# Performance work log

Measured on AMD Instinct MI355X. Metric: run time of the kernel, lower is better.

Reference implementation:

```python
import jax, jax.numpy as jnp
import numpy as np

H = 64; W = 64; P = 16; NPH = 4; NPW = 4; PH = 16; PW = 16; ZD = 32; HD = 1024; UD = 3; B = 256


def affine_grid(theta, Ho, Wo):
    # torch F.affine_grid, align_corners=False. theta [N,2,3] -> grid [N,Ho,Wo,2]
    xs = (2.0 * jnp.arange(Wo, dtype=theta.dtype) + 1.0) / Wo - 1.0
    ys = (2.0 * jnp.arange(Ho, dtype=theta.dtype) + 1.0) / Ho - 1.0
    X, Y = jnp.meshgrid(xs, ys)  # [Ho,Wo] each, x varies along last axis
    base = jnp.stack([X, Y, jnp.ones_like(X)], axis=-1)  # [Ho,Wo,3]
    return jnp.einsum('nij,hwj->nhwi', theta, base)


def grid_sample(img, grid):
    # torch F.grid_sample bilinear, padding_mode='zeros', align_corners=False
    # img [N,H,W], grid [N,Ho,Wo,2] in [-1,1]
    Hi, Wi = img.shape[1], img.shape[2]
    x = (grid[..., 0] + 1.0) * Wi / 2.0 - 0.5
    y = (grid[..., 1] + 1.0) * Hi / 2.0 - 0.5
    x0 = jnp.floor(x); y0 = jnp.floor(y)
    wx = x - x0; wy = y - y0

    def gather(ix, iy):
        valid = (ix >= 0) & (ix < Wi) & (iy >= 0) & (iy < Hi)
        ixc = jnp.clip(ix, 0, Wi - 1).astype(jnp.int32)
        iyc = jnp.clip(iy, 0, Hi - 1).astype(jnp.int32)
        v = jax.vmap(lambda im, yy, xx: im[yy, xx])(img, iyc, ixc)
        return jnp.where(valid, v, 0.0)

    return (gather(x0, y0) * (1 - wx) * (1 - wy)
            + gather(x0 + 1, y0) * wx * (1 - wy)
            + gather(x0, y0 + 1) * (1 - wx) * wy
            + gather(x0 + 1, y0 + 1) * wx * wy)


def rot_tr(u):
    # rotTrMatrix: u [N,3] (angle, tx, ty) -> [N,2,3]
    c = jnp.cos(u[:, 0]); s = jnp.sin(u[:, 0])
    R = jnp.stack([jnp.stack([c, -s], -1), jnp.stack([s, c], -1)], -2)  # [N,2,2]
    return jnp.concatenate([R, u[:, 1:3, None]], axis=2)


def anchor_theta():
    # anchor_move: identity rotation + per-part grid-cell-center translations
    tx = (np.arange(NPW) * (W / NPW) + W / NPW / 2) / W - 0.5
    ty = (np.arange(NPH) * (H / NPH) + H / NPH / 2) / H - 0.5
    th = np.tile(np.concatenate([np.eye(2), np.zeros((2, 1))], axis=1)[None], (P, 1, 1)).astype(np.float32)
    for k in range(P):
        th[k, 0, 2] = tx[k % NPW]
        th[k, 1, 2] = ty[k // NPW]
    return jnp.asarray(th)


def forward(inputs, W1, b1, W2, b2, Wum, bum, Wuv, buv, Wgm, bgm, Wgv, bgv, Wz, M, eps_u, eps_g):
    hid = jax.nn.relu(inputs.reshape(-1, H * W) @ W1 + b1)
    hid = jax.nn.relu(hid @ W2 + b2)
    # global transform distribution (note: F.threshold(x,-6,6) -> 6 where x<=-6)
    gmu = jnp.tanh(hid @ Wgm + bgm)
    gpre = hid @ Wgv + bgv
    gvar = jnp.exp(jnp.where(gpre > -6.0, gpre, 6.0))
    gu = gmu + gvar * eps_g  # sample_u uses mu + var*eps (var, not std) as in source
    # per-part transform distribution (F.threshold(x,-6,-6) -> clamp below at -6)
    umu = jnp.tanh(hid @ Wum + bum)
    upre = hid @ Wuv + buv
    uvar = jnp.exp(jnp.where(upre > -6.0, upre, -6.0))
    u = (umu + uvar * eps_u).reshape(-1, UD)  # [B*P,3]
    # decode parts (input is ones, as in source)
    parts = jax.nn.sigmoid(jnp.ones((B, ZD), inputs.dtype) @ Wz).reshape(B * P, PH, PW)
    padh = (H - PH) // 2; padw = (W - PW) // 2
    parts = jnp.pad(parts, ((0, 0), (padh, H - PH - padh), (padw, W - PW - padw)))
    # anchor placement of parts and kernel masks
    th_a = jnp.tile(anchor_theta(), (B, 1, 1))  # [B*P,2,3], part-minor ordering
    g_a = affine_grid(th_a, H, W)
    parts = grid_sample(parts, g_a)                     # [B*P,H,W]
    KM = grid_sample(M[:B * P].reshape(B * P, H, W), g_a)
    # per-part rotation+translation for parts; translation-only for kernel
    theta = rot_tr(u)                                   # [B*P,2,3]
    g = affine_grid(theta, H, W)
    eye = jnp.broadcast_to(jnp.eye(2, dtype=theta.dtype), (B * P, 2, 2))
    theta_K = jnp.concatenate([eye, theta[:, :, 2:3]], axis=2)
    g_K = affine_grid(theta_K, H, W)
    KM = grid_sample(KM, g_K).reshape(B, P, H, W)
    xp = grid_sample(parts, g).reshape(B, P, H, W)
    # masked weighted compositing
    num = jnp.sum(xp * KM, axis=1)
    den = jnp.sum(KM, axis=1)
    den = jnp.where(den == 0.0, 1.0, den)
    x = num / den
    # global transform
    theta_g = rot_tr(gu)
    g_g = affine_grid(theta_g, H, W)
    return grid_sample(x, g_g)[:, None]  # [B,1,H,W]


def setup_inputs() -> dict:
    key = jax.random.key(0)
    ks = jax.random.split(key, 18)

    def lin(k, fin, fout):
        return jax.random.normal(k, (fin, fout), jnp.float32) / np.sqrt(fin)

    return {
        'inputs': jax.random.uniform(ks[0], (B, H * W), jnp.float32),
        'W1': lin(ks[1], H * W, HD), 'b1': jnp.zeros((HD,), jnp.float32),
        'W2': lin(ks[2], HD, HD), 'b2': jnp.zeros((HD,), jnp.float32),
        'Wum': lin(ks[3], HD, P * UD), 'bum': jnp.zeros((P * UD,), jnp.float32),
        'Wuv': lin(ks[4], HD, P * UD), 'buv': jnp.zeros((P * UD,), jnp.float32),
        'Wgm': lin(ks[5], HD, UD), 'bgm': jnp.zeros((UD,), jnp.float32),
        'Wgv': lin(ks[6], HD, UD), 'bgv': jnp.zeros((UD,), jnp.float32),
        'Wz': lin(ks[7], ZD, P * PH * PW),
        'M': jax.random.uniform(ks[8], (B * P, 1, H, W), jnp.float32),
        'eps_u': jax.random.normal(ks[9], (B, P * UD), jnp.float32),
        'eps_g': jax.random.normal(ks[10], (B, UD), jnp.float32),
    }


def reference(inputs, W1, b1, W2, b2, Wum, bum, Wuv, buv, Wgm, bgm, Wgv, bgv, Wz, M, eps_u, eps_g):
    return forward(inputs, W1, b1, W2, b2, Wum, bum, Wuv, buv, Wgm, bgm, Wgv, bgv, Wz, M, eps_u, eps_g)
```

## Files before the change

### kernel.cpp

```cpp
#include <hip/hip_runtime.h>
#include <math.h>

#define SPLITK 8

typedef __bf16 bf16x8 __attribute__((ext_vector_type(8)));
typedef float  f32x4  __attribute__((ext_vector_type(4)));

__device__ inline unsigned short bf16rne(float x) {
    unsigned int u = __float_as_uint(x);
    unsigned int r = u + 0x7FFFu + ((u >> 16) & 1u);
    return (unsigned short)(r >> 16);
}
__device__ inline float bf16tof(unsigned short h) {
    return __uint_as_float(((unsigned int)h) << 16);
}

__global__ __launch_bounds__(256) void prep_all(
    const float* __restrict__ inputs,
    const float* __restrict__ W1, const float* __restrict__ W2,
    const float* __restrict__ Wum, const float* __restrict__ Wuv,
    const float* __restrict__ Wgm, const float* __restrict__ Wgv,
    const float* __restrict__ Wz,
    unsigned short* __restrict__ Ahi, unsigned short* __restrict__ Alo,
    unsigned short* __restrict__ W1Thi, unsigned short* __restrict__ W1Tlo,
    unsigned short* __restrict__ W2Thi, unsigned short* __restrict__ W2Tlo,
    float* __restrict__ WT, float* __restrict__ partsb)
{
    __shared__ float t[32][33];
    int bid = blockIdx.x;
    int tid = threadIdx.x;
    if (bid < 4096 || (bid >= 8192 && bid < 9216)) {
        const float* W = (bid < 4096) ? W1 : W2;
        unsigned short* Thi = (bid < 4096) ? W1Thi : W2Thi;
        unsigned short* Tlo = (bid < 4096) ? W1Tlo : W2Tlo;
        int K = (bid < 4096) ? 4096 : 1024;
        int b2 = (bid < 4096) ? bid : (bid - 8192);
        int n0 = (b2 & 31) * 32, k0 = (b2 >> 5) * 32;
        int c = tid & 31, r0 = tid >> 5;
#pragma unroll
        for (int i = 0; i < 4; i++)
            t[r0 + 8 * i][c] = W[(size_t)(k0 + r0 + 8 * i) * 1024 + n0 + c];
        __syncthreads();
        int kk = tid & 31, n1 = tid >> 5;
#pragma unroll
        for (int i = 0; i < 4; i++) {
            float x = t[kk][n1 + 8 * i];
            unsigned short h = bf16rne(x);
            unsigned short l = bf16rne(x - bf16tof(h));
            size_t o = (size_t)(n0 + n1 + 8 * i) * K + k0 + kk;
            Thi[o] = h;
            Tlo[o] = l;
        }
    } else if (bid < 8192) {
        int id = (bid - 4096) * 256 + tid;
        float x = inputs[id];
        unsigned short h = bf16rne(x);
        Ahi[id] = h;
        Alo[id] = bf16rne(x - bf16tof(h));
    } else if (bid < 9624) {
        int id = (bid - 9216) * 256 + tid;
        int o = id >> 10;
        int k = id & 1023;
        float v;
        if (o < 48)       v = Wum[k * 48 + o];
        else if (o < 96)  v = Wuv[k * 48 + (o - 48)];
        else if (o < 99)  v = Wgm[k * 3 + (o - 96)];
        else              v = Wgv[k * 3 + (o - 99)];
        WT[id] = v;
    } else {
        int idx = (bid - 9624) * 256 + tid;
        float s = 0.f;
#pragma unroll
        for (int z = 0; z < 32; z++) s += Wz[z * 4096 + idx];
        partsb[idx] = 1.f / (1.f + expf(-s));
    }
}

__global__ __launch_bounds__(256) void gemm_bf16x3(
    const unsigned short* __restrict__ Ahi, const unsigned short* __restrict__ Alo,
    const unsigned short* __restrict__ Bhi, const unsigned short* __restrict__ Blo,
    float* __restrict__ psum, int K, int kchunk)
{
    __shared__ unsigned short Ah[4096], Al[4096], Bh[4096], Bl[4096];
    int tid = threadIdx.x;
    int n0 = blockIdx.x * 64, m0 = blockIdx.y * 64;
    int kb = blockIdx.z * kchunk;
    int wid = tid >> 6, lane = tid & 63;
    int wm = wid & 1, wn = wid >> 1;
    int lm = lane & 15, q = lane >> 4;

    int r0 = tid >> 3, ch0 = tid & 7;
    int r1 = (tid + 256) >> 3, ch1 = (tid + 256) & 7;
    int l0 = r0 * 64 + 8 * (ch0 ^ (r0 & 7));
    int l1 = r1 * 64 + 8 * (ch1 ^ (r1 & 7));
    size_t ga0 = (size_t)(m0 + r0) * K + kb + ch0 * 8;
    size_t ga1 = (size_t)(m0 + r1) * K + kb + ch1 * 8;
    size_t gb0 = (size_t)(n0 + r0) * K + kb + ch0 * 8;
    size_t gb1 = (size_t)(n0 + r1) * K + kb + ch1 * 8;

    f32x4 acc[2][2] = {};

    int nkt = kchunk >> 6;
    uint4 vah0, vah1, val0, val1, vbh0, vbh1, vbl0, vbl1;
    vah0 = *(const uint4*)(Ahi + ga0);
    vah1 = *(const uint4*)(Ahi + ga1);
    val0 = *(const uint4*)(Alo + ga0);
    val1 = *(const uint4*)(Alo + ga1);
    vbh0 = *(const uint4*)(Bhi + gb0);
    vbh1 = *(const uint4*)(Bhi + gb1);
    vbl0 = *(const uint4*)(Blo + gb0);
    vbl1 = *(const uint4*)(Blo + gb1);

    int frm0 = (wm * 32 + lm) * 64;
    int frm1 = (wm * 32 + 16 + lm) * 64;
    int frn0 = (wn * 32 + lm) * 64;
    int frn1 = (wn * 32 + 16 + lm) * 64;
    int sw = lm & 7;

    for (int kt = 0; kt < nkt; kt++) {
        __syncthreads();
        *(uint4*)(Ah + l0) = vah0;
        *(uint4*)(Ah + l1) = vah1;
        *(uint4*)(Al + l0) = val0;
        *(uint4*)(Al + l1) = val1;
        *(uint4*)(Bh + l0) = vbh0;
        *(uint4*)(Bh + l1) = vbh1;
        *(uint4*)(Bl + l0) = vbl0;
        *(uint4*)(Bl + l1) = vbl1;
        __syncthreads();
        if (kt + 1 < nkt) {
            size_t o = (size_t)(kt + 1) * 64;
            vah0 = *(const uint4*)(Ahi + ga0 + o);
            vah1 = *(const uint4*)(Ahi + ga1 + o);
            val0 = *(const uint4*)(Alo + ga0 + o);
            val1 = *(const uint4*)(Alo + ga1 + o);
            vbh0 = *(const uint4*)(Bhi + gb0 + o);
            vbh1 = *(const uint4*)(Bhi + gb1 + o);
            vbl0 = *(const uint4*)(Blo + gb0 + o);
            vbl1 = *(const uint4*)(Blo + gb1 + o);
        }
#pragma unroll
        for (int ks = 0; ks < 2; ks++) {
            int cidx = 8 * (((ks << 2) + q) ^ sw);
            bf16x8 ah0 = *(const bf16x8*)(Ah + frm0 + cidx);
            bf16x8 ah1 = *(const bf16x8*)(Ah + frm1 + cidx);
            bf16x8 al0 = *(const bf16x8*)(Al + frm0 + cidx);
            bf16x8 al1 = *(const bf16x8*)(Al + frm1 + cidx);
            bf16x8 bh0 = *(const bf16x8*)(Bh + frn0 + cidx);
            bf16x8 bh1 = *(const bf16x8*)(Bh + frn1 + cidx);
            bf16x8 bl0 = *(const bf16x8*)(Bl + frn0 + cidx);
            bf16x8 bl1 = *(const bf16x8*)(Bl + frn1 + cidx);
            acc[0][0] = __builtin_amdgcn_mfma_f32_16x16x32_bf16(ah0, bh0, acc[0][0], 0, 0, 0);
            acc[0][0] = __builtin_amdgcn_mfma_f32_16x16x32_bf16(ah0, bl0, acc[0][0], 0, 0, 0);
            acc[0][0] = __builtin_amdgcn_mfma_f32_16x16x32_bf16(al0, bh0, acc[0][0], 0, 0, 0);
            acc[0][1] = __builtin_amdgcn_mfma_f32_16x16x32_bf16(ah0, bh1, acc[0][1], 0, 0, 0);
            acc[0][1] = __builtin_amdgcn_mfma_f32_16x16x32_bf16(ah0, bl1, acc[0][1], 0, 0, 0);
            acc[0][1] = __builtin_amdgcn_mfma_f32_16x16x32_bf16(al0, bh1, acc[0][1], 0, 0, 0);
            acc[1][0] = __builtin_amdgcn_mfma_f32_16x16x32_bf16(ah1, bh0, acc[1][0], 0, 0, 0);
            acc[1][0] = __builtin_amdgcn_mfma_f32_16x16x32_bf16(ah1, bl0, acc[1][0], 0, 0, 0);
            acc[1][0] = __builtin_amdgcn_mfma_f32_16x16x32_bf16(al1, bh0, acc[1][0], 0, 0, 0);
            acc[1][1] = __builtin_amdgcn_mfma_f32_16x16x32_bf16(ah1, bh1, acc[1][1], 0, 0, 0);
            acc[1][1] = __builtin_amdgcn_mfma_f32_16x16x32_bf16(ah1, bl1, acc[1][1], 0, 0, 0);
            acc[1][1] = __builtin_amdgcn_mfma_f32_16x16x32_bf16(al1, bh1, acc[1][1], 0, 0, 0);
        }
    }

    float* op = psum + (size_t)blockIdx.z * (256 * 1024);
#pragma unroll
    for (int mt = 0; mt < 2; mt++)
#pragma unroll
        for (int nt = 0; nt < 2; nt++) {
            int row = m0 + wm * 32 + mt * 16 + q * 4;
            int col = n0 + wn * 32 + nt * 16 + lm;
#pragma unroll
            for (int r = 0; r < 4; r++)
                op[(size_t)(row + r) * 1024 + col] = acc[mt][nt][r];
        }
}

__global__ __launch_bounds__(256) void reduce_bias_relu(
    const float* __restrict__ psum, const float* __restrict__ bias,
    float* __restrict__ out)
{
    int i = blockIdx.x * 256 + threadIdx.x;
    float v = 0.f;
#pragma unroll
    for (int s = 0; s < SPLITK; s++) v += psum[(size_t)s * 262144 + i];
    v += bias[i & 1023];
    out[i] = fmaxf(v, 0.f);
}

__global__ __launch_bounds__(256) void reduce_bias_relu_split(
    const float* __restrict__ psum, const float* __restrict__ bias,
    unsigned short* __restrict__ hi, unsigned short* __restrict__ lo)
{
    int i = blockIdx.x * 256 + threadIdx.x;
    float v = 0.f;
#pragma unroll
    for (int s = 0; s < SPLITK; s++) v += psum[(size_t)s * 262144 + i];
    v += bias[i & 1023];
    v = fmaxf(v, 0.f);
    unsigned short h = bf16rne(v);
    hi[i] = h;
    lo[i] = bf16rne(v - bf16tof(h));
}

__global__ __launch_bounds__(512) void heads_v2(
    const float* __restrict__ hid, const float* __restrict__ WT,
    const float* __restrict__ bum, const float* __restrict__ buv,
    const float* __restrict__ bgm, const float* __restrict__ bgv,
    const float* __restrict__ eps_u, const float* __restrict__ eps_g,
    float* __restrict__ u_out, float* __restrict__ gu_out)
{
    int b = blockIdx.x;
    int tid = threadIdx.x;
    int w = tid >> 6, l = tid & 63;

    const float* hp = hid + b * 1024 + l * 4;
    float4 hr[4];
#pragma unroll
    for (int i = 0; i < 4; i++) hr[i] = *(const float4*)(hp + i * 256);

    int o = w;
    int rm = (o < 48) ? o : (48 + o);
    int rv = (o < 48) ? (o + 48) : (51 + o);
    float4 wm[4], wv[4];
    {
        const float* wp = WT + rm * 1024 + l * 4;
#pragma unroll
        for (int i = 0; i < 4; i++) wm[i] = *(const float4*)(wp + i * 256);
        wp = WT + rv * 1024 + l * 4;
#pragma unroll
        for (int i = 0; i < 4; i++) wv[i] = *(const float4*)(wp + i * 256);
    }

    while (o < 51) {
        int onext = o + 8;
        float4 wmn[4], wvn[4];
        if (onext < 51) {
            int rm2 = (onext < 48) ? onext : (48 + onext);
            int rv2 = (onext < 48) ? (onext + 48) : (51 + onext);
            const float* wp = WT + rm2 * 1024 + l * 4;
#pragma unroll
            for (int i = 0; i < 4; i++) wmn[i] = *(const float4*)(wp + i * 256);
            wp = WT + rv2 * 1024 + l * 4;
#pragma unroll
            for (int i = 0; i < 4; i++) wvn[i] = *(const float4*)(wp + i * 256);
        }
        float am = 0.f, av = 0.f;
#pragma unroll
        for (int i = 0; i < 4; i++) {
            am = fmaf(hr[i].x, wm[i].x, am);
            am = fmaf(hr[i].y, wm[i].y, am);
            am = fmaf(hr[i].z, wm[i].z, am);
            am = fmaf(hr[i].w, wm[i].w, am);
            av = fmaf(hr[i].x, wv[i].x, av);
            av = fmaf(hr[i].y, wv[i].y, av);
            av = fmaf(hr[i].z, wv[i].z, av);
            av = fmaf(hr[i].w, wv[i].w, av);
        }
#pragma unroll
        for (int s = 32; s; s >>= 1) {
            am += __shfl_xor(am, s, 64);
            av += __shfl_xor(av, s, 64);
        }
        if (l == 0) {
            if (o < 48) {
                float umu = tanhf(am + bum[o]);
                float uvar = expf(fmaxf(av + buv[o], -6.f));
                u_out[b * 48 + o] = umu + uvar * eps_u[b * 48 + o];
            } else {
                int n = o - 48;
                float gmu = tanhf(am + bgm[n]);
                float gpre = av + bgv[n];
                float gvar = expf(gpre > -6.f ? gpre : 6.f);
                gu_out[b * 3 + n] = gmu + gvar * eps_g[b * 3 + n];
            }
        }
#pragma unroll
        for (int i = 0; i < 4; i++) { wm[i] = wmn[i]; wv[i] = wvn[i]; }
        o = onext;
    }
}

__global__ __launch_bounds__(256) void composite_v5(
    const float* __restrict__ M, const float* __restrict__ parts,
    const float* __restrict__ u, float* __restrict__ xout)
{
    __shared__ float patch[4096];
    __shared__ float plane[33 * 64];
    __shared__ float pc[16], psn[16], ptx[16], pty[16];
    int b = blockIdx.x >> 1;
    int half = blockIdx.x & 1;
    int tid = threadIdx.x;
    int brow0 = half * 32;

    for (int i = tid; i < 4096; i += 256) patch[i] = parts[i];
    if (tid < 16) {
        const float* up = u + (b * 16 + tid) * 3;
        float ang = up[0];
        pc[tid] = cosf(ang);
        psn[tid] = sinf(ang);
        ptx[tid] = up[1];
        pty[tid] = up[2];
    }
    __syncthreads();

    int j = tid & 63;
    int i0 = brow0 + (tid >> 6) * 8;
    float xnv = (float)(2 * j + 1) * (1.f / 64.f) - 1.f;

    float num[8] = {}, den[8] = {};
    const float* Mb = M + ((size_t)(b * 16) << 12);

    auto calc_iy = [&](int p, int& iy, int& iY, float& wy) {
        int dy = 8 * (p >> 2) - 12;
        float ay = fminf(fmaxf(32.f * pty[p], -16384.f), 16384.f);
        float fay = floorf(ay);
        wy = ay - fay;
        iy = (int)fay;
        iY = iy + dy;
    };

    int iy_c, iY_c; float wy_c;
    calc_iy(0, iy_c, iY_c, wy_c);
    float4 pf0, pf1, pf2;
    {
        const float* Mp = Mb;
        int lo = brow0 + iY_c;
        int rr0 = tid >> 4,           c0 = tid & 15;
        int rr1 = (tid + 256) >> 4,   c1 = (tid + 256) & 15;
        int rr2 = (tid + 512) >> 4,   c2 = (tid + 512) & 15;
        pf0 = *(const float4*)(Mp + (min(max(lo + rr0, 0), 63) << 6) + c0 * 4);
        pf1 = *(const float4*)(Mp + (min(max(lo + rr1, 0), 63) << 6) + c1 * 4);
        if (tid < 16)
            pf2 = *(const float4*)(Mp + (min(max(lo + rr2, 0), 63) << 6) + c2 * 4);
    }

    for (int p = 0; p < 16; p++) {
        {
            float4* dst = (float4*)plane;
            dst[tid] = pf0;
            dst[tid + 256] = pf1;
            if (tid < 16) dst[tid + 512] = pf2;
        }
        __syncthreads();
        int iy = iy_c, iY = iY_c; float wy = wy_c;
        if (p < 15) {
            calc_iy(p + 1, iy_c, iY_c, wy_c);
            const float* Mp = Mb + ((size_t)(p + 1) << 12);
            int lo = brow0 + iY_c;
            int rr0 = tid >> 4,           c0 = tid & 15;
            int rr1 = (tid + 256) >> 4,   c1 = (tid + 256) & 15;
            int rr2 = (tid + 512) >> 4,   c2 = (tid + 512) & 15;
            pf0 = *(const float4*)(Mp + (min(max(lo + rr0, 0), 63) << 6) + c0 * 4);
            pf1 = *(const float4*)(Mp + (min(max(lo + rr1, 0), 63) << 6) + c1 * 4);
            if (tid < 16)
                pf2 = *(const float4*)(Mp + (min(max(lo + rr2, 0), 63) << 6) + c2 * 4);
        }

        int dx = 8 * (p & 3) - 12;
        float c = pc[p], s = psn[p], tx = ptx[p];

        float ax = fminf(fmaxf(32.f * tx, -16384.f), 16384.f);
        float fax = floorf(ax);
        float wx = ax - fax;
        int ix = (int)fax;

        int x0 = j + ix;
        int X = x0 + dx;
        bool vc0 = ((unsigned)x0 < 64u) && ((unsigned)X < 64u);
        bool vc1 = ((unsigned)(x0 + 1) < 64u) && ((unsigned)(X + 1) < 64u);
        float w0 = vc0 ? (1.f - wx) : 0.f;
        float w1 = vc1 ? wx : 0.f;
        int Xc0 = min(max(X, 0), 63);
        int Xc1 = min(max(X + 1, 0), 63);

        float R[9];
#pragma unroll
        for (int r = 0; r < 9; r++) {
            int i = i0 + r;
            int y0i = i + iy;
            int ri = i + iY;
            bool vr = ((unsigned)y0i < 64u) && ((unsigned)ri < 64u);
            int lrow = (tid >> 6) * 8 + r;
            const float* row = plane + (lrow << 6);
            float val = fmaf(w0, row[Xc0], w1 * row[Xc1]);
            R[r] = vr ? val : 0.f;
        }

        float Ax = fmaf(c, xnv, tx);
        float Ay = fmaf(s, xnv, pty[p]);
        int ox = 24 - dx, oy = 24 - (8 * (p >> 2) - 12);
        const float* pp = patch + (p << 8);
#pragma unroll
        for (int r = 0; r < 8; r++) {
            int i = i0 + r;
            float km = fmaf(wy, R[r + 1] - R[r], R[r]);
            den[r] += km;

            float ynv = (float)(2 * i + 1) * (1.f / 64.f) - 1.f;
            float gx = fmaf(-s, ynv, Ax);
            float gy = fmaf(c, ynv, Ay);
            gx = fminf(fmaxf(gx, -8.f), 8.f);
            gy = fminf(fmaxf(gy, -8.f), 8.f);
            float xs = fmaf(gx, 32.f, 31.5f);
            float ysv = fmaf(gy, 32.f, 31.5f);
            float xf = floorf(xs), yf = floorf(ysv);
            float wxx = xs - xf, wyy = ysv - yf;
            int a0 = (int)yf - oy;
            int b0c = (int)xf - ox;
            if ((unsigned)(a0 + 1) <= 16u && (unsigned)(b0c + 1) <= 16u) {
                float v00 = 0.f, v10 = 0.f, v01 = 0.f, v11 = 0.f;
                if ((unsigned)a0 < 16u) {
                    const float* pr = pp + a0 * 16;
                    if ((unsigned)b0c < 16u) v00 = pr[b0c];
                    if ((unsigned)(b0c + 1) < 16u) v10 = pr[b0c + 1];
                }
                if ((unsigned)(a0 + 1) < 16u) {
                    const float* pr = pp + (a0 + 1) * 16;
                    if ((unsigned)b0c < 16u) v01 = pr[b0c];
                    if ((unsigned)(b0c + 1) < 16u) v11 = pr[b0c + 1];
                }
                float top = fmaf(wxx, v10 - v00, v00);
                float bot = fmaf(wxx, v11 - v01, v01);
                float xp = fmaf(wyy, bot - top, top);
                num[r] = fmaf(xp, km, num[r]);
            }
        }
        __syncthreads();
    }

    float* xo = xout + ((size_t)b << 12);
#pragma unroll
    for (int r = 0; r < 8; r++) {
        float d = (den[r] == 0.f) ? 1.f : den[r];
        xo[(i0 + r) * 64 + j] = num[r] / d;
    }
}

__global__ __launch_bounds__(256) void final_kernel(
    const float* __restrict__ xin, const float* __restrict__ gu,
    float* __restrict__ out)
{
    int id = blockIdx.x * 256 + threadIdx.x;
    int b = id >> 12;
    int pix = id & 4095;
    int ii = pix >> 6, jj = pix & 63;
    float ang = gu[b * 3 + 0], tx = gu[b * 3 + 1], ty = gu[b * 3 + 2];
    float c = cosf(ang), s = sinf(ang);
    float xn = (float)(2 * jj + 1) * (1.f / 64.f) - 1.f;
    float yn = (float)(2 * ii + 1) * (1.f / 64.f) - 1.f;
    float gx = c * xn - s * yn + tx;
    float gy = s * xn + c * yn + ty;
    float xs = (gx + 1.f) * 32.f - 0.5f;
    float ysv = (gy + 1.f) * 32.f - 0.5f;
    float xf = floorf(xs), yf = floorf(ysv);
    float wx = xs - xf, wy = ysv - yf;
    int x0 = (int)xf, y0 = (int)yf;
    const float* xp = xin + ((size_t)b << 12);
    float v00 = 0.f, v10 = 0.f, v01 = 0.f, v11 = 0.f;
    bool vx0 = (unsigned)x0 < 64u, vx1 = (unsigned)(x0 + 1) < 64u;
    if ((unsigned)y0 < 64u) {
        if (vx0) v00 = xp[y0 * 64 + x0];
        if (vx1) v10 = xp[y0 * 64 + x0 + 1];
    }
    if ((unsigned)(y0 + 1) < 64u) {
        if (vx0) v01 = xp[(y0 + 1) * 64 + x0];
        if (vx1) v11 = xp[(y0 + 1) * 64 + x0 + 1];
    }
    out[id] = v00 * (1.f - wx) * (1.f - wy) + v10 * wx * (1.f - wy)
            + v01 * (1.f - wx) * wy + v11 * wx * wy;
}

extern "C" void kernel_launch(void* const* d_in, const int* in_sizes, int n_in,
                              void* d_out, int out_size, void* d_ws, size_t ws_size,
                              hipStream_t stream)
{
    (void)in_sizes; (void)n_in; (void)out_size; (void)ws_size;
    const float* inputs = (const float*)d_in[0];
    const float* W1  = (const float*)d_in[1];
    const float* b1  = (const float*)d_in[2];
    const float* W2  = (const float*)d_in[3];
    const float* b2  = (const float*)d_in[4];
    const float* Wum = (const float*)d_in[5];
    const float* bum = (const float*)d_in[6];
    const float* Wuv = (const float*)d_in[7];
    const float* buv = (const float*)d_in[8];
    const float* Wgm = (const float*)d_in[9];
    const float* bgm = (const float*)d_in[10];
    const float* Wgv = (const float*)d_in[11];
    const float* bgv = (const float*)d_in[12];
    const float* Wz  = (const float*)d_in[13];
    const float* Mm  = (const float*)d_in[14];
    const float* eps_u = (const float*)d_in[15];
    const float* eps_g = (const float*)d_in[16];

    float* ws = (float*)d_ws;
    float* psum      = ws;
    float* hid2      = ws + 2097152;
    float* x_buf     = ws + 2359296;
    float* u_buf     = ws + 3407872;
    float* gu_buf    = ws + 3420160;
    float* parts_buf = ws + 3420928;
    float* WTh_buf   = ws + 3425024;
    unsigned short* us = (unsigned short*)(ws + 3529472);
    unsigned short* Ahi   = us;
    unsigned short* Alo   = Ahi + 1048576;
    unsigned short* W1Thi = Alo + 1048576;
    unsigned short* W1Tlo = W1Thi + 4194304;
    unsigned short* W2Thi = W1Tlo + 4194304;
    unsigned short* W2Tlo = W2Thi + 1048576;
    unsigned short* H1hi  = W2Tlo + 1048576;
    unsigned short* H1lo  = H1hi + 262144;

    prep_all<<<9640, 256, 0, stream>>>(inputs, W1, W2, Wum, Wuv, Wgm, Wgv, Wz,
                                       Ahi, Alo, W1Thi, W1Tlo, W2Thi, W2Tlo,
                                       WTh_buf, parts_buf);

    gemm_bf16x3<<<dim3(16, 4, SPLITK), 256, 0, stream>>>(Ahi, Alo, W1Thi, W1Tlo,
                                                         psum, 4096, 4096 / SPLITK);
    reduce_bias_relu_split<<<1024, 256, 0, stream>>>(psum, b1, H1hi, H1lo);
    gemm_bf16x3<<<dim3(16, 4, SPLITK), 256, 0, stream>>>(H1hi, H1lo, W2Thi, W2Tlo,
                                                         psum, 1024, 1024 / SPLITK);
    reduce_bias_relu<<<1024, 256, 0, stream>>>(psum, b2, hid2);
    heads_v2<<<256, 512, 0, stream>>>(hid2, WTh_buf, bum, buv, bgm, bgv,
                                      eps_u, eps_g, u_buf, gu_buf);
    composite_v5<<<512, 256, 0, stream>>>(Mm, parts_buf, u_buf, x_buf);
    final_kernel<<<4096, 256, 0, stream>>>(x_buf, gu_buf, (float*)d_out);
}
```

Measured before the change: 221.6 us.

## Split composite into quarter-image blocks with double-buffered plane staging

The composite kernel now assigns 16 rows per block instead of 32, doubling the grid to 1024 blocks. The shared-memory plane is double-buffered, so there is one barrier per part instead of two, and mask loads are prefetched two parts ahead. This aims to raise occupancy and overlap global loads with compute. In exchange, each block reloads the 4096-float patch and the part parameters, twice as many blocks now do so in total, and more mask halo rows are re-read.

New measurement: 210.2 us. 1.05x faster.

```diff
diff --git a/kernel.cpp b/kernel.cpp
--- a/kernel.cpp
+++ b/kernel.cpp
@@ -283,17 +283,17 @@
     }
 }
 
-__global__ __launch_bounds__(256) void composite_v5(
+__global__ __launch_bounds__(256) void composite_v6(
     const float* __restrict__ M, const float* __restrict__ parts,
     const float* __restrict__ u, float* __restrict__ xout)
 {
     __shared__ float patch[4096];
-    __shared__ float plane[33 * 64];
+    __shared__ float plane[2][17 * 64];
     __shared__ float pc[16], psn[16], ptx[16], pty[16];
-    int b = blockIdx.x >> 1;
-    int half = blockIdx.x & 1;
+    int b = blockIdx.x >> 2;
+    int quarter = blockIdx.x & 3;
     int tid = threadIdx.x;
-    int brow0 = half * 32;
+    int brow0 = quarter * 16;
 
     for (int i = tid; i < 4096; i += 256) patch[i] = parts[i];
     if (tid < 16) {
@@ -307,10 +307,10 @@
     __syncthreads();
 
     int j = tid & 63;
-    int i0 = brow0 + (tid >> 6) * 8;
+    int i0 = brow0 + (tid >> 6) * 4;
     float xnv = (float)(2 * j + 1) * (1.f / 64.f) - 1.f;
 
-    float num[8] = {}, den[8] = {};
+    float num[4] = {}, den[4] = {};
     const float* Mb = M + ((size_t)(b * 16) << 12);
 
     auto calc_iy = [&](int p, int& iy, int& iY, float& wy) {
@@ -322,43 +322,49 @@
         iY = iy + dy;
     };
 
-    int iy_c, iY_c; float wy_c;
-    calc_iy(0, iy_c, iY_c, wy_c);
-    float4 pf0, pf1, pf2;
+    int rr0 = tid >> 4, c0 = tid & 15;
+    int rr1 = (tid + 256) >> 4, c1 = (tid + 256) & 15;
+
+    int iy_arr[17], iY_arr[17]; float wy_arr[17];
+#pragma unroll
+    for (int p = 0; p < 16; p++) calc_iy(p, iy_arr[p], iY_arr[p], wy_arr[p]);
+
+    float4 pfA0, pfA1;
     {
-        const float* Mp = Mb;
-        int lo = brow0 + iY_c;
-        int rr0 = tid >> 4,           c0 = tid & 15;
-        int rr1 = (tid + 256) >> 4,   c1 = (tid + 256) & 15;
-        int rr2 = (tid + 512) >> 4,   c2 = (tid + 512) & 15;
-        pf0 = *(const float4*)(Mp + (min(max(lo + rr0, 0), 63) << 6) + c0 * 4);
-        pf1 = *(const float4*)(Mp + (min(max(lo + rr1, 0), 63) << 6) + c1 * 4);
+        int lo = brow0 + iY_arr[0];
+        pfA0 = *(const float4*)(Mb + (min(max(lo + rr0, 0), 63) << 6) + c0 * 4);
         if (tid < 16)
-            pf2 = *(const float4*)(Mp + (min(max(lo + rr2, 0), 63) << 6) + c2 * 4);
-    }
+            pfA1 = *(const float4*)(Mb + (min(max(lo + rr1, 0), 63) << 6) + c1 * 4);
+        float4* dst = (float4*)plane[0];
+        dst[tid] = pfA0;
+        if (tid < 16) dst[tid + 256] = pfA1;
+    }
+    {
+        int lo = brow0 + iY_arr[1];
+        const float* Mp = Mb + (1 << 12);
+        pfA0 = *(const float4*)(Mp + (min(max(lo + rr0, 0), 63) << 6) + c0 * 4);
+        if (tid < 16)
+            pfA1 = *(const float4*)(Mp + (min(max(lo + rr1, 0), 63) << 6) + c1 * 4);
+    }
+    __syncthreads();
 
     for (int p = 0; p < 16; p++) {
-        {
-            float4* dst = (float4*)plane;
-            dst[tid] = pf0;
-            dst[tid + 256] = pf1;
-            if (tid < 16) dst[tid + 512] = pf2;
-        }
-        __syncthreads();
-        int iy = iy_c, iY = iY_c; float wy = wy_c;
-        if (p < 15) {
-            calc_iy(p + 1, iy_c, iY_c, wy_c);
-            const float* Mp = Mb + ((size_t)(p + 1) << 12);
-            int lo = brow0 + iY_c;
-            int rr0 = tid >> 4,           c0 = tid & 15;
-            int rr1 = (tid + 256) >> 4,   c1 = (tid + 256) & 15;
-            int rr2 = (tid + 512) >> 4,   c2 = (tid + 512) & 15;
-            pf0 = *(const float4*)(Mp + (min(max(lo + rr0, 0), 63) << 6) + c0 * 4);
-            pf1 = *(const float4*)(Mp + (min(max(lo + rr1, 0), 63) << 6) + c1 * 4);
+        int cur = p & 1;
+        if (p + 1 < 16) {
+            float4* dst = (float4*)plane[1 - cur];
+            dst[tid] = pfA0;
+            if (tid < 16) dst[tid + 256] = pfA1;
+        }
+        if (p + 2 < 16) {
+            int lo = brow0 + iY_arr[p + 2];
+            const float* Mp = Mb + ((size_t)(p + 2) << 12);
+            pfA0 = *(const float4*)(Mp + (min(max(lo + rr0, 0), 63) << 6) + c0 * 4);
             if (tid < 16)
-                pf2 = *(const float4*)(Mp + (min(max(lo + rr2, 0), 63) << 6) + c2 * 4);
-        }
-
+                pfA1 = *(const float4*)(Mp + (min(max(lo + rr1, 0), 63) << 6) + c1 * 4);
+        }
+
+        int iy = iy_arr[p], iY = iY_arr[p];
+        float wy = wy_arr[p];
         int dx = 8 * (p & 3) - 12;
         float c = pc[p], s = psn[p], tx = ptx[p];
 
@@ -376,15 +382,16 @@
         int Xc0 = min(max(X, 0), 63);
         int Xc1 = min(max(X + 1, 0), 63);
 
-        float R[9];
-#pragma unroll
-        for (int r = 0; r < 9; r++) {
+        const float* pl = plane[cur];
+        float R[5];
+#pragma unroll
+        for (int r = 0; r < 5; r++) {
             int i = i0 + r;
             int y0i = i + iy;
             int ri = i + iY;
             bool vr = ((unsigned)y0i < 64u) && ((unsigned)ri < 64u);
-            int lrow = (tid >> 6) * 8 + r;
-            const float* row = plane + (lrow << 6);
+            int lrow = (tid >> 6) * 4 + r;
+            const float* row = pl + (lrow << 6);
             float val = fmaf(w0, row[Xc0], w1 * row[Xc1]);
             R[r] = vr ? val : 0.f;
         }
@@ -394,7 +401,7 @@
         int ox = 24 - dx, oy = 24 - (8 * (p >> 2) - 12);
         const float* pp = patch + (p << 8);
 #pragma unroll
-        for (int r = 0; r < 8; r++) {
+        for (int r = 0; r < 4; r++) {
             int i = i0 + r;
             float km = fmaf(wy, R[r + 1] - R[r], R[r]);
             den[r] += km;
@@ -433,7 +440,7 @@
 
     float* xo = xout + ((size_t)b << 12);
 #pragma unroll
-    for (int r = 0; r < 8; r++) {
+    for (int r = 0; r < 4; r++) {
         float d = (den[r] == 0.f) ? 1.f : den[r];
         xo[(i0 + r) * 64 + j] = num[r] / d;
     }
@@ -526,6 +533,6 @@
     reduce_bias_relu<<<1024, 256, 0, stream>>>(psum, b2, hid2);
     heads_v2<<<256, 512, 0, stream>>>(hid2, WTh_buf, bum, buv, bgm, bgv,
                                       eps_u, eps_g, u_buf, gu_buf);
-    composite_v5<<<512, 256, 0, stream>>>(Mm, parts_buf, u_buf, x_buf);
+    composite_v6<<<1024, 256, 0, stream>>>(Mm, parts_buf, u_buf, x_buf);
     final_kernel<<<4096, 256, 0, stream>>>(x_buf, gu_buf, (float*)d_out);
 }
```
